# Performance work log

Measured on AMD Instinct MI355X. Metric: run time of the kernel, lower is better.

## Reference

```python
import jax, jax.numpy as jnp
import numpy as np
from jax.ops import segment_sum, segment_max

N, H, E, NEXP, K, L, HEADS, NM = 384, 768, 12288, 8, 2, 3, 4, 38
GAMMA, LAMBDA_SPD = 2.0, 0.5


def _ln(x, g, b, eps=1e-5):
    m = jnp.mean(x, -1, keepdims=True)
    v = jnp.mean((x - m) ** 2, -1, keepdims=True)
    return (x - m) / jnp.sqrt(v + eps) * g + b


def _gelu(x):
    return jax.nn.gelu(x, approximate=False)


def setup_inputs() -> dict:
    key = jax.random.key(0)
    ks = jax.random.split(key, 20)
    r = lambda i, sh: jax.random.normal(ks[i], sh, jnp.float32) * 0.02
    z = lambda sh: jnp.zeros(sh, jnp.float32)
    o = lambda sh: jnp.ones(sh, jnp.float32)
    return dict(
        feat_text=jax.random.normal(ks[0], (N, H), jnp.float32),
        feat_image=jax.random.normal(ks[1], (N, H), jnp.float32),
        spd_matrix=jax.random.uniform(ks[2], (N, N), dtype=jnp.float32),
        src=jax.random.randint(ks[3], (E,), 0, N, jnp.int32),
        dst=jax.random.randint(ks[4], (E,), 0, N, jnp.int32),
        mask_idx=jax.random.randint(ks[5], (NM,), 0, N, jnp.int32),
        mask_token=r(6, (H,)),
        gate_W=r(7, (H, NEXP)), gate_b=z((NEXP,)),
        exp_W1=r(8, (NEXP, H, H)), exp_b1=z((NEXP, H)),
        exp_g1=o((NEXP, H)), exp_be1=z((NEXP, H)),
        exp_W2=r(9, (NEXP, H, H)), exp_b2=z((NEXP, H)),
        gat_W=r(10, (L, H, HEADS * H)), gat_al=r(11, (L, HEADS, H)),
        gat_ar=r(12, (L, HEADS, H)), gat_b=z((L, HEADS * H)),
        dec_W1=r(13, (2, H, H)), dec_b1=z((2, H)),
        dec_g=o((2, H)), dec_be=z((2, H)),
        dec_W2=r(14, (2, H, H)), dec_b2=z((2, H)),
        spd_W1=r(15, (2 * H, H)), spd_b1=z((H,)),
        spd_g=o((H,)), spd_be=z((H,)),
        spd_W2=r(16, (H, 1)), spd_b2=z((1,)),
    )


def _forward(feat_text, feat_image, spd_matrix, mask_token, gate_W, gate_b,
             exp_W1, exp_b1, exp_g1, exp_be1, exp_W2, exp_b2,
             gat_W, gat_al, gat_ar, gat_b,
             dec_W1, dec_b1, dec_g, dec_be, dec_W2, dec_b2,
             spd_W1, spd_b1, spd_g, spd_be, spd_W2, spd_b2,
             src, dst, mask_idx):
    # mean of domain features, then mask-token replacement at fixed indices
    x = (feat_text + feat_image) * 0.5
    xm = x.at[mask_idx].set(mask_token)

    # --- MoE (all experts computed densely, top-2 gathered, as in source) ---
    gw = jax.nn.softmax(xm @ gate_W + gate_b, axis=-1)              # [N,NEXP]
    topw, topi = jax.lax.top_k(gw, K)
    topw = topw / jnp.sum(topw, -1, keepdims=True)
    eh = _gelu(_ln(jnp.einsum('nd,edh->neh', xm, exp_W1) + exp_b1, exp_g1, exp_be1))
    eo = jnp.einsum('neh,ehk->nek', eh, exp_W2) + exp_b2            # [N,NEXP,H]
    sel = jnp.take_along_axis(eo, topi[:, :, None], axis=1)          # [N,K,H]
    h = jnp.sum(sel * topw[:, :, None], axis=1)                      # [N,H]

    # --- stacked GATConv layers (DGL semantics), head-mean after each ---
    for l in range(L):
        f = (h @ gat_W[l]).reshape(N, HEADS, H)                      # [N,heads,H]
        el = jnp.sum(f * gat_al[l], -1)                              # [N,heads]
        er = jnp.sum(f * gat_ar[l], -1)
        e = jax.nn.leaky_relu(el[src] + er[dst], 0.2)                # [E,heads]
        emax = segment_max(e, dst, num_segments=N)
        emax = jnp.where(jnp.isfinite(emax), emax, 0.0)
        ex = jnp.exp(e - emax[dst])
        den = segment_sum(ex, dst, num_segments=N)
        alpha = ex / jnp.maximum(den[dst], 1e-9)                     # edge softmax by dst
        rst = segment_sum(alpha[:, :, None] * f[src], dst, num_segments=N)
        h = jnp.mean(rst + gat_b[l].reshape(HEADS, H), axis=1)       # [N,H]

    # --- domain reconstruction loss on masked nodes ---
    hm = h[mask_idx]
    feats = (feat_text, feat_image)
    recon = jnp.float32(0.0)
    for d in range(2):
        zz = _gelu(_ln(hm @ dec_W1[d] + dec_b1[d], dec_g[d], dec_be[d]))
        rec = zz @ dec_W2[d] + dec_b2[d]
        orig = feats[d][mask_idx]
        denom = jnp.maximum(jnp.linalg.norm(rec, axis=-1) * jnp.linalg.norm(orig, axis=-1), 1e-8)
        cos = jnp.sum(rec * orig, -1) / denom
        recon = recon + jnp.mean((1.0 - cos) ** GAMMA)

    # --- SPD loss over all N^2 pairs, vectorized ---
    # concat([h_i, h_j]) @ W1 == h_i @ W1[:H] + h_j @ W1[H:]  (exact decomposition)
    pa = h @ spd_W1[:H]                                              # [N,H]
    pb = h @ spd_W1[H:]                                              # [N,H]
    zp = _gelu(_ln(pa[:, None, :] + pb[None, :, :] + spd_b1, spd_g, spd_be))  # [N,N,H]
    pred = (zp @ spd_W2)[..., 0] + spd_b2[0]                         # [N,N]
    spd_loss = jnp.mean((pred - spd_matrix) ** 2)

    total = recon + LAMBDA_SPD * spd_loss
    return total, h


def reference(feat_text, feat_image, spd_matrix, src, dst, mask_idx, mask_token,
              gate_W, gate_b, exp_W1, exp_b1, exp_g1, exp_be1, exp_W2, exp_b2,
              gat_W, gat_al, gat_ar, gat_b,
              dec_W1, dec_b1, dec_g, dec_be, dec_W2, dec_b2,
              spd_W1, spd_b1, spd_g, spd_be, spd_W2, spd_b2):
    return _forward(feat_text, feat_image, spd_matrix, mask_token, gate_W, gate_b,
                    exp_W1, exp_b1, exp_g1, exp_be1, exp_W2, exp_b2,
                    gat_W, gat_al, gat_ar, gat_b,
                    dec_W1, dec_b1, dec_g, dec_be, dec_W2, dec_b2,
                    spd_W1, spd_b1, spd_g, spd_be, spd_W2, spd_b2,
                    src, dst, mask_idx)
```

## Files before the change

kernel.cpp:

```cpp
#include <hip/hip_runtime.h>
#include <hip/hip_bf16.h>
#include <math.h>

#define NN 384
#define HD 768
#define EE 12288
#define NCHUNK (EE / 256)
#define NEXPERT 8
#define TOPK 2
#define NLAYER 3
#define NHEADS 4
#define NMASK 38

typedef __attribute__((ext_vector_type(8))) short short8v;
typedef __attribute__((ext_vector_type(4))) float f32x4;
typedef __attribute__((ext_vector_type(2))) float f32x2;
typedef __attribute__((ext_vector_type(4))) int int4v;

__device__ __forceinline__ float gelu_f(float x) {
    return x * 0.5f * (1.f + erff(x * 0.70710678118654752440f));
}

__device__ __forceinline__ ushort f2bf(float x) {
    unsigned u = __float_as_uint(x);
    u += 0x7fffu + ((u >> 16) & 1u);
    return (ushort)(u >> 16);
}

__global__ __launch_bounds__(256) void k_xm_gate(const float* __restrict__ a,
        const float* __restrict__ b, const int* __restrict__ mask_idx,
        const float* __restrict__ mt, ushort* __restrict__ xm_bf,
        const float* __restrict__ gW, const float* __restrict__ gb,
        int* __restrict__ topi, float* __restrict__ topw) {
    int n = blockIdx.x, tid = threadIdx.x;
    __shared__ float xs[HD];
    __shared__ int ism;
    __shared__ float logits[NEXPERT];
    if (tid == 0) ism = 0;
    __syncthreads();
    if (tid < NMASK && mask_idx[tid] == n) ism = 1;
    __syncthreads();
#pragma unroll
    for (int r = 0; r < 3; r++) {
        int j = r * 256 + tid;
        float v = ism ? mt[j] : 0.5f * (a[(size_t)n * HD + j] + b[(size_t)n * HD + j]);
        xs[j] = v;
        xm_bf[(size_t)n * HD + j] = f2bf(v);
    }
    __syncthreads();
    int grp = tid >> 5;
    int l32 = tid & 31;
    float p = 0.f;
    for (int dd = l32; dd < HD; dd += 32) p += xs[dd] * gW[dd * NEXPERT + grp];
#pragma unroll
    for (int m = 1; m < 32; m <<= 1) p += __shfl_xor(p, m, 32);
    if (l32 == 0) logits[grp] = p + gb[grp];
    __syncthreads();
    if (tid == 0) {
        float mx = logits[0];
#pragma unroll
        for (int e = 1; e < NEXPERT; e++) mx = fmaxf(mx, logits[e]);
        float sm[NEXPERT]; float s = 0.f;
#pragma unroll
        for (int e = 0; e < NEXPERT; e++) { sm[e] = expf(logits[e] - mx); s += sm[e]; }
#pragma unroll
        for (int e = 0; e < NEXPERT; e++) sm[e] /= s;
        int i0 = 0; float b0 = sm[0];
#pragma unroll
        for (int e = 1; e < NEXPERT; e++) if (sm[e] > b0) { b0 = sm[e]; i0 = e; }
        int i1 = -1; float b1v = -1.f;
#pragma unroll
        for (int e = 0; e < NEXPERT; e++) if (e != i0 && sm[e] > b1v) { b1v = sm[e]; i1 = e; }
        float ssum = b0 + b1v;
        topi[n * 2] = i0; topi[n * 2 + 1] = i1;
        topw[n * 2] = b0 / ssum; topw[n * 2 + 1] = b1v / ssum;
    }
}

__global__ __launch_bounds__(256) void k_transpose_all(
        const float* __restrict__ w1, const float* __restrict__ w2,
        const float* __restrict__ gw, const float* __restrict__ sw,
        const float* __restrict__ dw1, const float* __restrict__ dw2,
        ushort* __restrict__ o1, ushort* __restrict__ o2, ushort* __restrict__ og,
        ushort* __restrict__ os, ushort* __restrict__ od1, ushort* __restrict__ od2) {
    int b = blockIdx.x;
    const float* src; ushort* dst; int N, loc, tilesX;
    if (b < 4608)       { src = w1;  dst = o1;  N = HD;     loc = b;         tilesX = 24; }
    else if (b < 9216)  { src = w2;  dst = o2;  N = HD;     loc = b - 4608;  tilesX = 24; }
    else if (b < 16128) { src = gw;  dst = og;  N = 4 * HD; loc = b - 9216;  tilesX = 96; }
    else if (b < 17280) { src = sw;  dst = os;  N = HD;     loc = b - 16128; tilesX = 24; }
    else if (b < 18432) { src = dw1; dst = od1; N = HD;     loc = b - 17280; tilesX = 24; }
    else                { src = dw2; dst = od2; N = HD;     loc = b - 18432; tilesX = 24; }
    const int K = HD;
    int tilesPerZ = tilesX * 24;
    int z = loc / tilesPerZ;
    int rem = loc - z * tilesPerZ;
    int ty = rem / tilesX, tx = rem - ty * tilesX;
    const float* inz = src + (size_t)z * K * N;
    ushort* outz = dst + (size_t)z * K * N;
    int n0 = tx * 32, k0 = ty * 32;

    __shared__ float t[32][36];
    int r = threadIdx.x >> 3, c4 = (threadIdx.x & 7) * 4;
    float4 v = *reinterpret_cast<const float4*>(inz + (size_t)(k0 + r) * N + n0 + c4);
    t[r][c4] = v.x; t[r][c4 + 1] = v.y; t[r][c4 + 2] = v.z; t[r][c4 + 3] = v.w;
    __syncthreads();
    int orow = n0 + r;
    uint2 p;
    ushort b0 = f2bf(t[c4 + 0][r]);
    ushort b1 = f2bf(t[c4 + 1][r]);
    ushort b2 = f2bf(t[c4 + 2][r]);
    ushort b3 = f2bf(t[c4 + 3][r]);
    p.x = (unsigned)b0 | ((unsigned)b1 << 16);
    p.y = (unsigned)b2 | ((unsigned)b3 << 16);
    *reinterpret_cast<uint2*>(outz + (size_t)orow * K + k0 + c4) = p;
}

__global__ __launch_bounds__(256) void k_moe_meta(const int* __restrict__ topi,
        int* __restrict__ ecnt, int* __restrict__ estart, int* __restrict__ posArr,
        int* __restrict__ eofpos, int* __restrict__ rowlist, int* __restrict__ dec_rs) {
    __shared__ int ti[NN * TOPK];
    __shared__ int cnt[NEXPERT];
    __shared__ int est[NEXPERT + 1];
    int tid = threadIdx.x;
    if (tid < NEXPERT) cnt[tid] = 0;
    __syncthreads();
    for (int a = tid; a < NN * TOPK; a += 256) ti[a] = topi[a];
    __syncthreads();
    for (int a = tid; a < NN * TOPK; a += 256) atomicAdd(&cnt[ti[a]], 1);
    __syncthreads();
    if (tid == 0) {
        int s = 0;
        for (int e = 0; e < NEXPERT; e++) { est[e] = s; s += cnt[e]; }
        est[NEXPERT] = s;
        dec_rs[0] = 0; dec_rs[1] = NMASK;
    }
    __syncthreads();
    if (tid < NEXPERT) { ecnt[tid] = cnt[tid]; estart[tid] = est[tid]; }
    if (tid == 0) estart[NEXPERT] = est[NEXPERT];
    for (int a = tid; a < NN * TOPK; a += 256) {
        int e = ti[a]; int rank = 0;
        for (int a2 = 0; a2 < a; a2++) rank += (ti[a2] == e) ? 1 : 0;
        int p = est[e] + rank;
        posArr[a] = p; eofpos[p] = e; rowlist[p] = a >> 1;
    }
}

__global__ __launch_bounds__(256) void k_hist(const int* __restrict__ dst,
                                              int* __restrict__ counts) {
    __shared__ int h[NN];
    int c = blockIdx.x;
    for (int i = threadIdx.x; i < NN; i += 256) h[i] = 0;
    __syncthreads();
    atomicAdd(&h[dst[c * 256 + threadIdx.x]], 1);
    __syncthreads();
    for (int i = threadIdx.x; i < NN; i += 256) counts[c * NN + i] = h[i];
}

__global__ __launch_bounds__(NN) void k_scan_all(const int* __restrict__ counts,
        int* __restrict__ chunkbase, int* __restrict__ nstart) {
    __shared__ int tot[NN];
    int n = threadIdx.x;
    int s = 0;
    for (int c = 0; c < NCHUNK; c++) { chunkbase[c * NN + n] = s; s += counts[c * NN + n]; }
    tot[n] = s;
    __syncthreads();
    for (int off = 1; off < NN; off <<= 1) {
        int v = tot[n];
        int add = (n >= off) ? tot[n - off] : 0;
        __syncthreads();
        tot[n] = v + add;
        __syncthreads();
    }
    nstart[n + 1] = tot[n];
    if (n == 0) nstart[0] = 0;
}

__global__ __launch_bounds__(256) void k_rank2(const int* __restrict__ dst,
        const int* __restrict__ chunkbase, const int* __restrict__ nstart,
        int* __restrict__ esorted) {
    __shared__ int ds[256];
    int c = blockIdx.x;
    int e = c * 256 + threadIdx.x;
    int d = dst[e];
    ds[threadIdx.x] = d;
    __syncthreads();
    int r = 0;
    for (int i = 0; i < threadIdx.x; i++) r += (ds[i] == d) ? 1 : 0;
    esorted[nstart[d] + chunkbase[c * NN + d] + r] = e;
}

__device__ __forceinline__ short8v ldfrag(const ushort* s, int r, int kb) {
    int c = kb ^ (r & 7);
    return *reinterpret_cast<const short8v*>(s + r * 64 + c * 8);
}

__global__ __launch_bounds__(256) void k_mfma_gemm(
        const ushort* __restrict__ A, const ushort* __restrict__ Bt, float* __restrict__ C,
        int M, int K, int lda, int ldc, long strideBt, long strideC,
        const int* __restrict__ rowsA, const int* __restrict__ Ms,
        const int* __restrict__ rowStarts) {
    int z = blockIdx.z;
    int Meff = Ms ? Ms[z] : M;
    int row0 = blockIdx.y * 64;
    if (row0 >= Meff) return;
    int col0 = blockIdx.x * 64;
    int rowbase = rowStarts ? rowStarts[z] : 0;
    const ushort* Btz = Bt + (size_t)z * strideBt;
    float* Cz = C + (size_t)rowbase * ldc + (size_t)z * strideC;
    const int* rz = rowsA ? (rowsA + rowbase) : nullptr;

    __shared__ ushort Asm[64 * 64];
    __shared__ ushort Bsm[64 * 64];

    int tid = threadIdx.x;
    int w = tid >> 6, lane = tid & 63;
    int wr = w >> 1, wc = w & 1;
    int l15 = lane & 15, lq = lane >> 4;

    f32x4 acc[2][2];
#pragma unroll
    for (int i = 0; i < 2; i++)
#pragma unroll
        for (int j = 0; j < 2; j++) acc[i][j] = (f32x4){0.f, 0.f, 0.f, 0.f};

    for (int k0 = 0; k0 < K; k0 += 64) {
#pragma unroll
        for (int ii = 0; ii < 2; ii++) {
            int i = tid + ii * 256;
            int r = i >> 3, c = i & 7;
            int cs = c ^ (r & 7);
            int4v av = (int4v){0, 0, 0, 0};
            int grow = row0 + r;
            if (grow < Meff) {
                int srow = rz ? rz[grow] : (rowbase + grow);
                av = *reinterpret_cast<const int4v*>(A + (size_t)srow * lda + k0 + c * 8);
            }
            *reinterpret_cast<int4v*>(&Asm[r * 64 + cs * 8]) = av;
            int4v bv = *reinterpret_cast<const int4v*>(Btz + (size_t)(col0 + r) * K + k0 + c * 8);
            *reinterpret_cast<int4v*>(&Bsm[r * 64 + cs * 8]) = bv;
        }
        __syncthreads();
#pragma unroll
        for (int ks = 0; ks < 2; ks++) {
            int kb = ks * 4 + lq;
            short8v a0 = ldfrag(Asm, wr * 32 + l15, kb);
            short8v a1 = ldfrag(Asm, wr * 32 + 16 + l15, kb);
            short8v b0 = ldfrag(Bsm, wc * 32 + l15, kb);
            short8v b1 = ldfrag(Bsm, wc * 32 + 16 + l15, kb);
            acc[0][0] = __builtin_amdgcn_mfma_f32_16x16x32_bf16(a0, b0, acc[0][0], 0, 0, 0);
            acc[0][1] = __builtin_amdgcn_mfma_f32_16x16x32_bf16(a0, b1, acc[0][1], 0, 0, 0);
            acc[1][0] = __builtin_amdgcn_mfma_f32_16x16x32_bf16(a1, b0, acc[1][0], 0, 0, 0);
            acc[1][1] = __builtin_amdgcn_mfma_f32_16x16x32_bf16(a1, b1, acc[1][1], 0, 0, 0);
        }
        __syncthreads();
    }
#pragma unroll
    for (int ai = 0; ai < 2; ai++)
#pragma unroll
        for (int bi = 0; bi < 2; bi++) {
            int rbase = row0 + wr * 32 + ai * 16 + (lq << 2);
            int cc = col0 + wc * 32 + bi * 16 + l15;
#pragma unroll
            for (int r = 0; r < 4; r++) {
                int rr = rbase + r;
                if (rr < Meff) Cz[(size_t)rr * ldc + cc] = acc[ai][bi][r];
            }
        }
}

__global__ __launch_bounds__(256) void k_ln_gelu(const float* __restrict__ t1,
        ushort* __restrict__ ehb, const float* __restrict__ b1, const float* __restrict__ g,
        const float* __restrict__ be, const int* __restrict__ eofpos) {
    int row = blockIdx.x;
    int e = eofpos[row];
    int tid = threadIdx.x;
    __shared__ float rA[4], rB[4];
    float v[3]; float s1 = 0.f, s2 = 0.f;
#pragma unroll
    for (int r = 0; r < 3; r++) {
        int c = r * 256 + tid;
        float x = t1[(size_t)row * HD + c] + b1[e * HD + c];
        v[r] = x; s1 += x; s2 += x * x;
    }
#pragma unroll
    for (int m = 1; m < 64; m <<= 1) { s1 += __shfl_xor(s1, m); s2 += __shfl_xor(s2, m); }
    int wave = tid >> 6, lane = tid & 63;
    if (lane == 0) { rA[wave] = s1; rB[wave] = s2; }
    __syncthreads();
    float S1 = rA[0] + rA[1] + rA[2] + rA[3];
    float S2 = rB[0] + rB[1] + rB[2] + rB[3];
    float mean = S1 * (1.f / HD);
    float var = S2 * (1.f / HD) - mean * mean;
    float rstd = rsqrtf(var + 1e-5f);
#pragma unroll
    for (int r = 0; r < 3; r++) {
        int c = r * 256 + tid;
        float zn = (v[r] - mean) * rstd * g[e * HD + c] + be[e * HD + c];
        ehb[(size_t)row * HD + c] = f2bf(gelu_f(zn));
    }
}

__global__ void k_combine_moe(const float* __restrict__ eo, const float* __restrict__ b2,
        const int* __restrict__ topi, const float* __restrict__ topw,
        const int* __restrict__ posArr, float* __restrict__ h, ushort* __restrict__ hb) {
    int n = blockIdx.x;
    int tid = threadIdx.x;
    int e0 = topi[n * 2], e1 = topi[n * 2 + 1];
    float w0 = topw[n * 2], w1 = topw[n * 2 + 1];
    int p0 = posArr[n * 2], p1 = posArr[n * 2 + 1];
    for (int j = tid; j < HD; j += 256) {
        float v0 = eo[(size_t)p0 * HD + j] + b2[e0 * HD + j];
        float v1 = eo[(size_t)p1 * HD + j] + b2[e1 * HD + j];
        float hv = w0 * v0 + w1 * v1;
        h[(size_t)n * HD + j] = hv;
        hb[(size_t)n * HD + j] = f2bf(hv);
    }
}

__global__ __launch_bounds__(256) void k_el_er(const float* __restrict__ f,
        const float* __restrict__ al, const float* __restrict__ ar,
        float* __restrict__ el, float* __restrict__ er) {
    int n = blockIdx.x;
    int hd = threadIdx.x >> 6, lane = threadIdx.x & 63;
    const float* fr = f + ((size_t)n * NHEADS + hd) * HD;
    float pl = 0.f, pr = 0.f;
    for (int j = lane; j < HD; j += 64) {
        float fv = fr[j];
        pl += fv * al[hd * HD + j];
        pr += fv * ar[hd * HD + j];
    }
#pragma unroll
    for (int m = 1; m < 64; m <<= 1) { pl += __shfl_xor(pl, m); pr += __shfl_xor(pr, m); }
    if (lane == 0) { el[n * NHEADS + hd] = pl; er[n * NHEADS + hd] = pr; }
}

__global__ __launch_bounds__(256) void k_gat_agg(const float* __restrict__ f,
        const float* __restrict__ el, const float* __restrict__ er,
        const int* __restrict__ src, const int* __restrict__ esorted,
        const int* __restrict__ nstart, const float* __restrict__ gb,
        float* __restrict__ hout, ushort* __restrict__ hb) {
    int n = blockIdx.x;
    int s0 = nstart[n], cnt = nstart[n + 1] - s0;
    int tid = threadIdx.x;
    __shared__ float red[4][NHEADS];
    __shared__ float emax_s[NHEADS], den_s[NHEADS];
    __shared__ float alpha_s[256][NHEADS];
    __shared__ int sn_s[256];
    float ern[NHEADS];
#pragma unroll
    for (int hd = 0; hd < NHEADS; hd++) ern[hd] = er[n * NHEADS + hd];
    int wave = tid >> 6, lane = tid & 63;

    float mx[NHEADS] = { -1e30f, -1e30f, -1e30f, -1e30f };
    for (int t = tid; t < cnt; t += 256) {
        int e = esorted[s0 + t]; int sn = src[e];
#pragma unroll
        for (int hd = 0; hd < NHEADS; hd++) {
            float v = el[sn * NHEADS + hd] + ern[hd];
            v = (v >= 0.f) ? v : 0.2f * v;
            mx[hd] = fmaxf(mx[hd], v);
        }
    }
#pragma unroll
    for (int hd = 0; hd < NHEADS; hd++) {
#pragma unroll
        for (int m = 1; m < 64; m <<= 1) mx[hd] = fmaxf(mx[hd], __shfl_xor(mx[hd], m));
    }
    if (lane == 0) { for (int hd = 0; hd < NHEADS; hd++) red[wave][hd] = mx[hd]; }
    __syncthreads();
    if (tid == 0) {
#pragma unroll
        for (int hd = 0; hd < NHEADS; hd++)
            emax_s[hd] = fmaxf(fmaxf(red[0][hd], red[1][hd]), fmaxf(red[2][hd], red[3][hd]));
    }
    __syncthreads();
    float sm[NHEADS] = { 0.f, 0.f, 0.f, 0.f };
    for (int t = tid; t < cnt; t += 256) {
        int e = esorted[s0 + t]; int sn = src[e];
#pragma unroll
        for (int hd = 0; hd < NHEADS; hd++) {
            float v = el[sn * NHEADS + hd] + ern[hd];
            v = (v >= 0.f) ? v : 0.2f * v;
            sm[hd] += expf(v - emax_s[hd]);
        }
    }
#pragma unroll
    for (int hd = 0; hd < NHEADS; hd++) {
#pragma unroll
        for (int m = 1; m < 64; m <<= 1) sm[hd] += __shfl_xor(sm[hd], m);
    }
    __syncthreads();
    if (lane == 0) { for (int hd = 0; hd < NHEADS; hd++) red[wave][hd] = sm[hd]; }
    __syncthreads();
    if (tid == 0) {
#pragma unroll
        for (int hd = 0; hd < NHEADS; hd++)
            den_s[hd] = red[0][hd] + red[1][hd] + red[2][hd] + red[3][hd];
    }
    __syncthreads();
    float acc[NHEADS][3] = {};
    for (int c0 = 0; c0 < cnt; c0 += 256) {
        int t = c0 + tid;
        if (t < cnt) {
            int e = esorted[s0 + t]; int sn = src[e];
            sn_s[tid] = sn;
#pragma unroll
            for (int hd = 0; hd < NHEADS; hd++) {
                float v = el[sn * NHEADS + hd] + ern[hd];
                v = (v >= 0.f) ? v : 0.2f * v;
                alpha_s[tid][hd] = expf(v - emax_s[hd]) / fmaxf(den_s[hd], 1e-9f);
            }
        }
        __syncthreads();
        int cm = cnt - c0; if (cm > 256) cm = 256;
        for (int i = 0; i < cm; i++) {
            int sn = sn_s[i];
            const float* fr = f + (size_t)sn * (NHEADS * HD);
#pragma unroll
            for (int hd = 0; hd < NHEADS; hd++) {
                float a = alpha_s[i][hd];
#pragma unroll
                for (int r = 0; r < 3; r++) acc[hd][r] += a * fr[hd * HD + r * 256 + tid];
            }
        }
        __syncthreads();
    }
#pragma unroll
    for (int r = 0; r < 3; r++) {
        int j = r * 256 + tid;
        float s = 0.f;
#pragma unroll
        for (int hd = 0; hd < NHEADS; hd++) s += acc[hd][r] + gb[hd * HD + j];
        float hv = 0.25f * s;
        hout[(size_t)n * HD + j] = hv;
        hb[(size_t)n * HD + j] = f2bf(hv);
    }
}

__global__ __launch_bounds__(256) void k_ln_gelu_dec(const float* __restrict__ t1,
        ushort* __restrict__ zzb, const float* __restrict__ b1, const float* __restrict__ g,
        const float* __restrict__ be) {
    int m = blockIdx.x, d = blockIdx.y;
    int row = d * NMASK + m;
    int tid = threadIdx.x;
    __shared__ float rA[4], rB[4];
    float v[3]; float s1 = 0.f, s2 = 0.f;
#pragma unroll
    for (int r = 0; r < 3; r++) {
        int c = r * 256 + tid;
        float x = t1[(size_t)row * HD + c] + b1[d * HD + c];
        v[r] = x; s1 += x; s2 += x * x;
    }
#pragma unroll
    for (int mm = 1; mm < 64; mm <<= 1) { s1 += __shfl_xor(s1, mm); s2 += __shfl_xor(s2, mm); }
    int wave = tid >> 6, lane = tid & 63;
    if (lane == 0) { rA[wave] = s1; rB[wave] = s2; }
    __syncthreads();
    float S1 = rA[0] + rA[1] + rA[2] + rA[3];
    float S2 = rB[0] + rB[1] + rB[2] + rB[3];
    float mean = S1 * (1.f / HD);
    float var = S2 * (1.f / HD) - mean * mean;
    float rstd = rsqrtf(var + 1e-5f);
#pragma unroll
    for (int r = 0; r < 3; r++) {
        int c = r * 256 + tid;
        float zn = (v[r] - mean) * rstd * g[d * HD + c] + be[d * HD + c];
        zzb[(size_t)row * HD + c] = f2bf(gelu_f(zn));
    }
}

__global__ __launch_bounds__(256) void k_cos(const float* __restrict__ rec,
        const float* __restrict__ b2, const int* __restrict__ mask_idx,
        const float* __restrict__ ft, const float* __restrict__ fi,
        float* __restrict__ rec_part) {
    int b = blockIdx.x;
    int d = b / NMASK, m = b % NMASK;
    int node = mask_idx[m];
    int tid = threadIdx.x;
    __shared__ float rA[4], rB[4], rC[4];
    const float* rrow = rec + (size_t)b * HD;
    const float* orig = (d == 0 ? ft : fi) + (size_t)node * HD;
    float pro = 0.f, prr = 0.f, poo = 0.f;
#pragma unroll
    for (int r = 0; r < 3; r++) {
        int c = r * 256 + tid;
        float rv = rrow[c] + b2[d * HD + c];
        float o = orig[c];
        pro += rv * o; prr += rv * rv; poo += o * o;
    }
#pragma unroll
    for (int mm = 1; mm < 64; mm <<= 1) {
        pro += __shfl_xor(pro, mm); prr += __shfl_xor(prr, mm); poo += __shfl_xor(poo, mm);
    }
    int wave = tid >> 6, lane = tid & 63;
    if (lane == 0) { rA[wave] = pro; rB[wave] = prr; rC[wave] = poo; }
    __syncthreads();
    if (tid == 0) {
        float P = rA[0] + rA[1] + rA[2] + rA[3];
        float R = rB[0] + rB[1] + rB[2] + rB[3];
        float O = rC[0] + rC[1] + rC[2] + rC[3];
        float denom = fmaxf(sqrtf(R) * sqrtf(O), 1e-8f);
        float cosv = P / denom;
        float t = 1.f - cosv;
        rec_part[b] = (t * t) * (1.f / (float)NMASK);
    }
}

__global__ __launch_bounds__(256) void k_spd_prep(float* __restrict__ pab,
        const float* __restrict__ b1, ushort* __restrict__ pp_bf,
        float* __restrict__ Svec, float* __restrict__ Qvec) {
    int r = blockIdx.x, tid = threadIdx.x;
    bool isA = r < NN;
    float* row = pab + (size_t)r * HD;
    __shared__ float rA[4], rB[4];
    float vv[3]; float s1 = 0.f, s2 = 0.f;
#pragma unroll
    for (int rr = 0; rr < 3; rr++) {
        int j = rr * 256 + tid;
        float v = row[j];
        if (isA) v += b1[j];
        vv[rr] = v; s1 += v; s2 += v * v;
    }
#pragma unroll
    for (int m = 1; m < 64; m <<= 1) { s1 += __shfl_xor(s1, m); s2 += __shfl_xor(s2, m); }
    int wave = tid >> 6, lane = tid & 63;
    if (lane == 0) { rA[wave] = s1; rB[wave] = s2; }
#pragma unroll
    for (int rr = 0; rr < 3; rr++) {
        int j = rr * 256 + tid;
        if (isA) row[j] = vv[rr];
        pp_bf[(size_t)r * HD + j] = f2bf(vv[rr]);
    }
    __syncthreads();
    if (tid == 0) {
        Svec[r] = rA[0] + rA[1] + rA[2] + rA[3];
        Qvec[r] = rB[0] + rB[1] + rB[2] + rB[3];
    }
}

#define GC1 2.3022085f
#define GC2 0.10294429f
__global__ __launch_bounds__(256) void k_spd2(const float* __restrict__ pab,
        const float* __restrict__ Svec, const float* __restrict__ Qvec,
        const float* __restrict__ cross, const float* __restrict__ g,
        const float* __restrict__ be, const float* __restrict__ w2,
        const float* __restrict__ b2, const float* __restrict__ spd,
        float* __restrict__ partials) {
    __shared__ f32x2 pa_s[HD / 2], g_s[HD / 2], be_s[HD / 2], w2_s[HD / 2];
    __shared__ float wsum[4];
    int i = blockIdx.x;
    const f32x2* paP = reinterpret_cast<const f32x2*>(pab + (size_t)i * HD);
    const f32x2* gP = reinterpret_cast<const f32x2*>(g);
    const f32x2* beP = reinterpret_cast<const f32x2*>(be);
    const f32x2* w2P = reinterpret_cast<const f32x2*>(w2);
    for (int t = threadIdx.x; t < HD / 2; t += 256) {
        pa_s[t] = paP[t];
        g_s[t] = gP[t]; be_s[t] = beP[t]; w2_s[t] = w2P[t];
    }
    __syncthreads();
    int wave = threadIdx.x >> 6, lane = threadIdx.x & 63;
    float Sa = Svec[i], Qa = Qvec[i];
    float bacc = 0.f;
    float b2v = b2[0];
    for (int j = blockIdx.y * 4 + wave; j < NN; j += 32) {
        const f32x2* pbj = reinterpret_cast<const f32x2*>(pab + (size_t)(NN + j) * HD);
        float mean = (Sa + Svec[NN + j]) * (1.f / HD);
        float ex2 = (Qa + Qvec[NN + j] + 2.f * cross[(size_t)i * NN + j]) * (1.f / HD);
        float var = ex2 - mean * mean;
        float rstd = rsqrtf(var + 1e-5f);
        f32x2 rstd2 = (f32x2){rstd, rstd};
        float nmr = -mean * rstd;
        f32x2 nmr2 = (f32x2){nmr, nmr};
        f32x2 dot2 = (f32x2){0.f, 0.f};
#pragma unroll
        for (int r = 0; r < 6; r++) {
            int e = r * 64 + lane;
            f32x2 z = pa_s[e] + pbj[e];
            f32x2 u = z * rstd2 + nmr2;
            f32x2 zn = u * g_s[e] + be_s[e];
            f32x2 t2 = zn * zn;
            f32x2 p = t2 * (f32x2){GC2, GC2} + (f32x2){GC1, GC1};
            f32x2 ua = zn * p;
            float e0 = __builtin_amdgcn_exp2f(-ua.x);
            float e1 = __builtin_amdgcn_exp2f(-ua.y);
            f32x2 rr = (f32x2){__builtin_amdgcn_rcpf(1.f + e0),
                               __builtin_amdgcn_rcpf(1.f + e1)};
            f32x2 gl = zn * rr;
            dot2 = gl * w2_s[e] + dot2;
        }
        float dot = dot2.x + dot2.y;
#pragma unroll
        for (int m = 1; m < 64; m <<= 1) dot += __shfl_xor(dot, m);
        if (lane == 0) {
            float d = (dot + b2v) - spd[(size_t)i * NN + j];
            bacc += d * d;
        }
    }
    if (lane == 0) wsum[wave] = bacc;
    __syncthreads();
    if (threadIdx.x == 0) partials[i * 8 + blockIdx.y] = wsum[0] + wsum[1] + wsum[2] + wsum[3];
}

__global__ __launch_bounds__(256) void k_out(const float* __restrict__ h,
        const float* __restrict__ rec_part, const float* __restrict__ spd_part,
        float* __restrict__ out) {
    if (blockIdx.x < NN * HD / 256) {
        int i = blockIdx.x * 256 + threadIdx.x;
        out[1 + i] = h[i];
        return;
    }
    __shared__ float rA[4], rB[4];
    int tid = threadIdx.x;
    float sp = 0.f, rc = 0.f;
    for (int t = tid; t < 8 * NN; t += 256) sp += spd_part[t];
    for (int t = tid; t < 2 * NMASK; t += 256) rc += rec_part[t];
#pragma unroll
    for (int m = 1; m < 64; m <<= 1) { sp += __shfl_xor(sp, m); rc += __shfl_xor(rc, m); }
    int wave = tid >> 6, lane = tid & 63;
    if (lane == 0) { rA[wave] = sp; rB[wave] = rc; }
    __syncthreads();
    if (tid == 0) {
        float SP = rA[0] + rA[1] + rA[2] + rA[3];
        float RC = rB[0] + rB[1] + rB[2] + rB[3];
        out[0] = RC + 0.5f * (SP * (1.f / ((float)NN * (float)NN)));
    }
}

extern "C" void kernel_launch(void* const* d_in, const int* in_sizes, int n_in,
                              void* d_out, int out_size, void* d_ws, size_t ws_size,
                              hipStream_t stream) {
    const float* feat_text = (const float*)d_in[0];
    const float* feat_image = (const float*)d_in[1];
    const float* spd_matrix = (const float*)d_in[2];
    const int*   src       = (const int*)d_in[3];
    const int*   dst       = (const int*)d_in[4];
    const int*   mask_idx  = (const int*)d_in[5];
    const float* mask_token = (const float*)d_in[6];
    const float* gate_W = (const float*)d_in[7];
    const float* gate_b = (const float*)d_in[8];
    const float* exp_W1 = (const float*)d_in[9];
    const float* exp_b1 = (const float*)d_in[10];
    const float* exp_g1 = (const float*)d_in[11];
    const float* exp_be1 = (const float*)d_in[12];
    const float* exp_W2 = (const float*)d_in[13];
    const float* exp_b2 = (const float*)d_in[14];
    const float* gat_W  = (const float*)d_in[15];
    const float* gat_al = (const float*)d_in[16];
    const float* gat_ar = (const float*)d_in[17];
    const float* gat_b  = (const float*)d_in[18];
    const float* dec_W1 = (const float*)d_in[19];
    const float* dec_b1 = (const float*)d_in[20];
    const float* dec_g  = (const float*)d_in[21];
    const float* dec_be = (const float*)d_in[22];
    const float* dec_W2 = (const float*)d_in[23];
    const float* dec_b2 = (const float*)d_in[24];
    const float* spd_W1 = (const float*)d_in[25];
    const float* spd_b1 = (const float*)d_in[26];
    const float* spd_g  = (const float*)d_in[27];
    const float* spd_be = (const float*)d_in[28];
    const float* spd_W2 = (const float*)d_in[29];
    const float* spd_b2 = (const float*)d_in[30];
    (void)in_sizes; (void)n_in; (void)ws_size; (void)out_size;

    float* ws = (float*)d_ws;
    size_t off = 0;
    auto alloc = [&](size_t nfl) { float* p = ws + off; off += (nfl + 3) & ~(size_t)3; return p; };
    float* hA   = alloc((size_t)NN * HD);
    float* hB   = alloc((size_t)NN * HD);
    float* t1   = alloc((size_t)NN * TOPK * HD);
    float* eo   = alloc((size_t)NN * TOPK * HD);
    float* fbuf = alloc((size_t)NN * NHEADS * HD);
    float* el   = alloc(NN * NHEADS);
    float* er   = alloc(NN * NHEADS);
    float* pab  = alloc((size_t)2 * NN * HD);
    float* cross = alloc((size_t)NN * NN);
    float* Svec = alloc(2 * NN);
    float* Qvec = alloc(2 * NN);
    float* topw = alloc(NN * TOPK);
    float* rec_part = alloc(2 * NMASK + 4);
    float* spd_part = alloc(8 * NN);
    int* topi    = (int*)alloc(NN * TOPK);
    int* ecnt    = (int*)alloc(16);
    int* estart  = (int*)alloc(16);
    int* posArr  = (int*)alloc(NN * TOPK);
    int* eofpos  = (int*)alloc(NN * TOPK);
    int* rowlist = (int*)alloc(NN * TOPK);
    int* dec_rs  = (int*)alloc(4);
    int* nstart  = (int*)alloc(NN + 4);
    int* esorted = (int*)alloc(EE);
    int* counts    = (int*)alloc((size_t)NCHUNK * NN);
    int* chunkbase = (int*)alloc((size_t)NCHUNK * NN);
    ushort* xm_bf  = (ushort*)alloc((size_t)NN * HD / 2);
    ushort* eh_bf  = (ushort*)alloc((size_t)NN * TOPK * HD / 2);
    ushort* hA_bf  = (ushort*)alloc((size_t)NN * HD / 2);
    ushort* hB_bf  = (ushort*)alloc((size_t)NN * HD / 2);
    ushort* pp_bf  = (ushort*)alloc((size_t)2 * NN * HD / 2);
    ushort* expW1t = (ushort*)alloc((size_t)NEXPERT * HD * HD / 2);
    ushort* expW2t = (ushort*)alloc((size_t)NEXPERT * HD * HD / 2);
    ushort* gatWt  = (ushort*)alloc((size_t)NLAYER * NHEADS * HD * HD / 2);
    ushort* spdW1t = (ushort*)alloc((size_t)2 * HD * HD / 2);
    ushort* decW1t = (ushort*)alloc((size_t)2 * HD * HD / 2);
    ushort* decW2t = (ushort*)alloc((size_t)2 * HD * HD / 2);

    k_transpose_all<<<dim3(19584), dim3(256), 0, stream>>>(
        exp_W1, exp_W2, gat_W, spd_W1, dec_W1, dec_W2,
        expW1t, expW2t, gatWt, spdW1t, decW1t, decW2t);

    k_xm_gate<<<dim3(NN), dim3(256), 0, stream>>>(
        feat_text, feat_image, mask_idx, mask_token, xm_bf, gate_W, gate_b, topi, topw);
    k_moe_meta<<<dim3(1), dim3(256), 0, stream>>>(topi, ecnt, estart, posArr, eofpos,
                                                  rowlist, dec_rs);

    k_hist<<<dim3(NCHUNK), dim3(256), 0, stream>>>(dst, counts);
    k_scan_all<<<dim3(1), dim3(NN), 0, stream>>>(counts, chunkbase, nstart);
    k_rank2<<<dim3(NCHUNK), dim3(256), 0, stream>>>(dst, chunkbase, nstart, esorted);

    k_mfma_gemm<<<dim3(HD / 64, 12, NEXPERT), dim3(256), 0, stream>>>(
        xm_bf, expW1t, t1, 0, HD, HD, HD, (long)HD * HD, 0, rowlist, ecnt, estart);
    k_ln_gelu<<<dim3(NN * TOPK), dim3(256), 0, stream>>>(t1, eh_bf, exp_b1, exp_g1, exp_be1, eofpos);
    k_mfma_gemm<<<dim3(HD / 64, 12, NEXPERT), dim3(256), 0, stream>>>(
        eh_bf, expW2t, eo, 0, HD, HD, HD, (long)HD * HD, 0, nullptr, ecnt, estart);
    k_combine_moe<<<dim3(NN), dim3(256), 0, stream>>>(eo, exp_b2, topi, topw, posArr, hA, hA_bf);

    float* hcur = hA; float* hnxt = hB;
    ushort* hcur_bf = hA_bf; ushort* hnxt_bf = hB_bf;
    for (int l = 0; l < NLAYER; l++) {
        k_mfma_gemm<<<dim3(NHEADS * HD / 64, NN / 64, 1), dim3(256), 0, stream>>>(
            hcur_bf, gatWt + (size_t)l * NHEADS * HD * HD, fbuf,
            NN, HD, HD, NHEADS * HD, 0, 0, nullptr, nullptr, nullptr);
        k_el_er<<<dim3(NN), dim3(256), 0, stream>>>(
            fbuf, gat_al + (size_t)l * NHEADS * HD, gat_ar + (size_t)l * NHEADS * HD, el, er);
        k_gat_agg<<<dim3(NN), dim3(256), 0, stream>>>(
            fbuf, el, er, src, esorted, nstart, gat_b + (size_t)l * NHEADS * HD, hnxt, hnxt_bf);
        float* t = hcur; hcur = hnxt; hnxt = t;
        ushort* tb = hcur_bf; hcur_bf = hnxt_bf; hnxt_bf = tb;
    }

    k_mfma_gemm<<<dim3(HD / 64, 1, 2), dim3(256), 0, stream>>>(
        hcur_bf, decW1t, t1, NMASK, HD, HD, HD, (long)HD * HD, (long)NMASK * HD,
        mask_idx, nullptr, nullptr);
    k_ln_gelu_dec<<<dim3(NMASK, 2), dim3(256), 0, stream>>>(t1, eh_bf, dec_b1, dec_g, dec_be);
    k_mfma_gemm<<<dim3(HD / 64, 1, 2), dim3(256), 0, stream>>>(
        eh_bf, decW2t, eo, NMASK, HD, HD, HD, (long)HD * HD, 0,
        nullptr, nullptr, dec_rs);
    k_cos<<<dim3(2 * NMASK), dim3(256), 0, stream>>>(
        eo, dec_b2, mask_idx, feat_text, feat_image, rec_part);

    k_mfma_gemm<<<dim3(HD / 64, NN / 64, 2), dim3(256), 0, stream>>>(
        hcur_bf, spdW1t, pab, NN, HD, HD, HD, (long)HD * HD, (long)NN * HD,
        nullptr, nullptr, nullptr);
    k_spd_prep<<<dim3(2 * NN), dim3(256), 0, stream>>>(pab, spd_b1, pp_bf, Svec, Qvec);
    k_mfma_gemm<<<dim3(NN / 64, NN / 64, 1), dim3(256), 0, stream>>>(
        pp_bf, pp_bf + (size_t)NN * HD, cross, NN, HD, HD, NN, 0, 0,
        nullptr, nullptr, nullptr);
    k_spd2<<<dim3(NN, 8), dim3(256), 0, stream>>>(
        pab, Svec, Qvec, cross, spd_g, spd_be, spd_W2, spd_b2, spd_matrix, spd_part);

    k_out<<<dim3(NN * HD / 256 + 1), dim3(256), 0, stream>>>(
        hcur, rec_part, spd_part, (float*)d_out);
}
```

Baseline: 361.1 us.

## Restructure SPD pairwise kernel to thread-per-pair with transposed pb, use direct global-to-LDS loads in GEMM

The SPD pairwise GELU/LN kernel is rewritten so that each thread handles one (i,j) pair and iterates over the hidden dimension. It reads a transposed copy of pb written by the prep kernel, which gives coalesced column loads, and reads pa, gamma, beta and w2 packed as float4 from LDS. This replaces the per-pair wave reduction with one lane-level accumulation, removing the cross-lane shuffles per pair. The MFMA GEMM tile loads now use global_load_lds to copy straight into LDS, skipping the register staging. Out-of-range rows are clamped to Meff-1 instead of zero-filled. This adds an extra transposed buffer write.

```diff
diff --git a/kernel.cpp b/kernel.cpp
--- a/kernel.cpp
+++ b/kernel.cpp
@@ -14,7 +14,6 @@
 
 typedef __attribute__((ext_vector_type(8))) short short8v;
 typedef __attribute__((ext_vector_type(4))) float f32x4;
-typedef __attribute__((ext_vector_type(2))) float f32x2;
 typedef __attribute__((ext_vector_type(4))) int int4v;
 
 __device__ __forceinline__ float gelu_f(float x) {
@@ -25,6 +24,12 @@
     unsigned u = __float_as_uint(x);
     u += 0x7fffu + ((u >> 16) & 1u);
     return (ushort)(u >> 16);
+}
+
+__device__ __forceinline__ void gload_lds16(const void* g, void* l) {
+    __builtin_amdgcn_global_load_lds(
+        (const __attribute__((address_space(1))) void*)g,
+        (__attribute__((address_space(3))) void*)l, 16, 0, 0);
 }
 
 __global__ __launch_bounds__(256) void k_xm_gate(const float* __restrict__ a,
@@ -218,6 +223,7 @@
     int wr = w >> 1, wc = w & 1;
     int l15 = lane & 15, lq = lane >> 4;
 
+    int r0s = tid >> 3, c0s = tid & 7;
     f32x4 acc[2][2];
 #pragma unroll
     for (int i = 0; i < 2; i++)
@@ -227,18 +233,15 @@
     for (int k0 = 0; k0 < K; k0 += 64) {
 #pragma unroll
         for (int ii = 0; ii < 2; ii++) {
-            int i = tid + ii * 256;
-            int r = i >> 3, c = i & 7;
-            int cs = c ^ (r & 7);
-            int4v av = (int4v){0, 0, 0, 0};
+            int r = r0s + ii * 32;
+            int cs = c0s ^ (r & 7);
             int grow = row0 + r;
-            if (grow < Meff) {
-                int srow = rz ? rz[grow] : (rowbase + grow);
-                av = *reinterpret_cast<const int4v*>(A + (size_t)srow * lda + k0 + c * 8);
-            }
-            *reinterpret_cast<int4v*>(&Asm[r * 64 + cs * 8]) = av;
-            int4v bv = *reinterpret_cast<const int4v*>(Btz + (size_t)(col0 + r) * K + k0 + c * 8);
-            *reinterpret_cast<int4v*>(&Bsm[r * 64 + cs * 8]) = bv;
+            int gc = (grow < Meff) ? grow : (Meff - 1);
+            int srow = rz ? rz[gc] : (rowbase + gc);
+            ushort* ldsA = &Asm[(size_t)(w * 8 + ii * 32) * 64];
+            ushort* ldsB = &Bsm[(size_t)(w * 8 + ii * 32) * 64];
+            gload_lds16(A + (size_t)srow * lda + k0 + cs * 8, ldsA);
+            gload_lds16(Btz + (size_t)(col0 + r) * K + k0 + cs * 8, ldsB);
         }
         __syncthreads();
 #pragma unroll
@@ -509,7 +512,7 @@
 
 __global__ __launch_bounds__(256) void k_spd_prep(float* __restrict__ pab,
         const float* __restrict__ b1, ushort* __restrict__ pp_bf,
-        float* __restrict__ Svec, float* __restrict__ Qvec) {
+        float* __restrict__ Svec, float* __restrict__ Qvec, float* __restrict__ pbT) {
     int r = blockIdx.x, tid = threadIdx.x;
     bool isA = r < NN;
     float* row = pab + (size_t)r * HD;
@@ -530,6 +533,7 @@
     for (int rr = 0; rr < 3; rr++) {
         int j = rr * 256 + tid;
         if (isA) row[j] = vv[rr];
+        else pbT[(size_t)j * NN + (r - NN)] = vv[rr];
         pp_bf[(size_t)r * HD + j] = f2bf(vv[rr]);
     }
     __syncthreads();
@@ -541,65 +545,61 @@
 
 #define GC1 2.3022085f
 #define GC2 0.10294429f
-__global__ __launch_bounds__(256) void k_spd2(const float* __restrict__ pab,
-        const float* __restrict__ Svec, const float* __restrict__ Qvec,
-        const float* __restrict__ cross, const float* __restrict__ g,
-        const float* __restrict__ be, const float* __restrict__ w2,
-        const float* __restrict__ b2, const float* __restrict__ spd,
-        float* __restrict__ partials) {
-    __shared__ f32x2 pa_s[HD / 2], g_s[HD / 2], be_s[HD / 2], w2_s[HD / 2];
-    __shared__ float wsum[4];
+__device__ __forceinline__ float gfast(float zn) {
+    float ua = zn * fmaf(zn * zn, GC2, GC1);
+    float e = __builtin_amdgcn_exp2f(-ua);
+    return zn * __builtin_amdgcn_rcpf(1.f + e);
+}
+
+__global__ __launch_bounds__(384) void k_spdj(const float* __restrict__ pab,
+        const float* __restrict__ pbT, const float* __restrict__ Svec,
+        const float* __restrict__ Qvec, const float* __restrict__ cross,
+        const float* __restrict__ g, const float* __restrict__ be,
+        const float* __restrict__ w2, const float* __restrict__ b2,
+        const float* __restrict__ spd, float* __restrict__ partials) {
     int i = blockIdx.x;
-    const f32x2* paP = reinterpret_cast<const f32x2*>(pab + (size_t)i * HD);
-    const f32x2* gP = reinterpret_cast<const f32x2*>(g);
-    const f32x2* beP = reinterpret_cast<const f32x2*>(be);
-    const f32x2* w2P = reinterpret_cast<const f32x2*>(w2);
-    for (int t = threadIdx.x; t < HD / 2; t += 256) {
-        pa_s[t] = paP[t];
-        g_s[t] = gP[t]; be_s[t] = beP[t]; w2_s[t] = w2P[t];
-    }
-    __syncthreads();
-    int wave = threadIdx.x >> 6, lane = threadIdx.x & 63;
+    int wv = threadIdx.x >> 6, lane = threadIdx.x & 63;
+    int j = threadIdx.x;
+    __shared__ __align__(16) float PG[HD][4];
+    for (int t = threadIdx.x; t < HD; t += 384) {
+        PG[t][0] = pab[(size_t)i * HD + t];
+        PG[t][1] = g[t];
+        PG[t][2] = be[t];
+        PG[t][3] = w2[t];
+    }
+    __syncthreads();
     float Sa = Svec[i], Qa = Qvec[i];
-    float bacc = 0.f;
-    float b2v = b2[0];
-    for (int j = blockIdx.y * 4 + wave; j < NN; j += 32) {
-        const f32x2* pbj = reinterpret_cast<const f32x2*>(pab + (size_t)(NN + j) * HD);
-        float mean = (Sa + Svec[NN + j]) * (1.f / HD);
-        float ex2 = (Qa + Qvec[NN + j] + 2.f * cross[(size_t)i * NN + j]) * (1.f / HD);
-        float var = ex2 - mean * mean;
-        float rstd = rsqrtf(var + 1e-5f);
-        f32x2 rstd2 = (f32x2){rstd, rstd};
-        float nmr = -mean * rstd;
-        f32x2 nmr2 = (f32x2){nmr, nmr};
-        f32x2 dot2 = (f32x2){0.f, 0.f};
-#pragma unroll
-        for (int r = 0; r < 6; r++) {
-            int e = r * 64 + lane;
-            f32x2 z = pa_s[e] + pbj[e];
-            f32x2 u = z * rstd2 + nmr2;
-            f32x2 zn = u * g_s[e] + be_s[e];
-            f32x2 t2 = zn * zn;
-            f32x2 p = t2 * (f32x2){GC2, GC2} + (f32x2){GC1, GC1};
-            f32x2 ua = zn * p;
-            float e0 = __builtin_amdgcn_exp2f(-ua.x);
-            float e1 = __builtin_amdgcn_exp2f(-ua.y);
-            f32x2 rr = (f32x2){__builtin_amdgcn_rcpf(1.f + e0),
-                               __builtin_amdgcn_rcpf(1.f + e1)};
-            f32x2 gl = zn * rr;
-            dot2 = gl * w2_s[e] + dot2;
-        }
-        float dot = dot2.x + dot2.y;
-#pragma unroll
-        for (int m = 1; m < 64; m <<= 1) dot += __shfl_xor(dot, m);
-        if (lane == 0) {
-            float d = (dot + b2v) - spd[(size_t)i * NN + j];
-            bacc += d * d;
-        }
-    }
-    if (lane == 0) wsum[wave] = bacc;
-    __syncthreads();
-    if (threadIdx.x == 0) partials[i * 8 + blockIdx.y] = wsum[0] + wsum[1] + wsum[2] + wsum[3];
+    float mean = (Sa + Svec[NN + j]) * (1.f / HD);
+    float ex2 = (Qa + Qvec[NN + j] + 2.f * cross[(size_t)i * NN + j]) * (1.f / HD);
+    float rstd = rsqrtf(ex2 - mean * mean + 1e-5f);
+    float nmr = -mean * rstd;
+    const float* pcol = pbT + j;
+    float d0 = 0.f, d1 = 0.f, d2 = 0.f, d3 = 0.f;
+#pragma unroll 2
+    for (int e = 0; e < HD; e += 4) {
+        float p0 = pcol[(size_t)(e + 0) * NN];
+        float p1 = pcol[(size_t)(e + 1) * NN];
+        float p2 = pcol[(size_t)(e + 2) * NN];
+        float p3 = pcol[(size_t)(e + 3) * NN];
+        float4 q0 = *reinterpret_cast<const float4*>(&PG[e + 0][0]);
+        float4 q1 = *reinterpret_cast<const float4*>(&PG[e + 1][0]);
+        float4 q2 = *reinterpret_cast<const float4*>(&PG[e + 2][0]);
+        float4 q3 = *reinterpret_cast<const float4*>(&PG[e + 3][0]);
+        float zn0 = fmaf(fmaf(q0.x + p0, rstd, nmr), q0.y, q0.z);
+        float zn1 = fmaf(fmaf(q1.x + p1, rstd, nmr), q1.y, q1.z);
+        float zn2 = fmaf(fmaf(q2.x + p2, rstd, nmr), q2.y, q2.z);
+        float zn3 = fmaf(fmaf(q3.x + p3, rstd, nmr), q3.y, q3.z);
+        d0 = fmaf(gfast(zn0), q0.w, d0);
+        d1 = fmaf(gfast(zn1), q1.w, d1);
+        d2 = fmaf(gfast(zn2), q2.w, d2);
+        d3 = fmaf(gfast(zn3), q3.w, d3);
+    }
+    float pred = ((d0 + d1) + (d2 + d3)) + b2[0];
+    float diff = pred - spd[(size_t)i * NN + j];
+    float sq = diff * diff;
+#pragma unroll
+    for (int m = 1; m < 64; m <<= 1) sq += __shfl_xor(sq, m);
+    if (lane == 0) partials[i * 6 + wv] = sq;
 }
 
 __global__ __launch_bounds__(256) void k_out(const float* __restrict__ h,
@@ -613,7 +613,7 @@
     __shared__ float rA[4], rB[4];
     int tid = threadIdx.x;
     float sp = 0.f, rc = 0.f;
-    for (int t = tid; t < 8 * NN; t += 256) sp += spd_part[t];
+    for (int t = tid; t < 6 * NN; t += 256) sp += spd_part[t];
     for (int t = tid; t < 2 * NMASK; t += 256) rc += rec_part[t];
 #pragma unroll
     for (int m = 1; m < 64; m <<= 1) { sp += __shfl_xor(sp, m); rc += __shfl_xor(rc, m); }
@@ -674,12 +674,13 @@
     float* el   = alloc(NN * NHEADS);
     float* er   = alloc(NN * NHEADS);
     float* pab  = alloc((size_t)2 * NN * HD);
+    float* pbT  = alloc((size_t)HD * NN);
     float* cross = alloc((size_t)NN * NN);
     float* Svec = alloc(2 * NN);
     float* Qvec = alloc(2 * NN);
     float* topw = alloc(NN * TOPK);
     float* rec_part = alloc(2 * NMASK + 4);
-    float* spd_part = alloc(8 * NN);
+    float* spd_part = alloc(6 * NN);
     int* topi    = (int*)alloc(NN * TOPK);
     int* ecnt    = (int*)alloc(16);
     int* estart  = (int*)alloc(16);
@@ -750,12 +751,12 @@
     k_mfma_gemm<<<dim3(HD / 64, NN / 64, 2), dim3(256), 0, stream>>>(
         hcur_bf, spdW1t, pab, NN, HD, HD, HD, (long)HD * HD, (long)NN * HD,
         nullptr, nullptr, nullptr);
-    k_spd_prep<<<dim3(2 * NN), dim3(256), 0, stream>>>(pab, spd_b1, pp_bf, Svec, Qvec);
+    k_spd_prep<<<dim3(2 * NN), dim3(256), 0, stream>>>(pab, spd_b1, pp_bf, Svec, Qvec, pbT);
     k_mfma_gemm<<<dim3(NN / 64, NN / 64, 1), dim3(256), 0, stream>>>(
         pp_bf, pp_bf + (size_t)NN * HD, cross, NN, HD, HD, NN, 0, 0,
         nullptr, nullptr, nullptr);
-    k_spd2<<<dim3(NN, 8), dim3(256), 0, stream>>>(
-        pab, Svec, Qvec, cross, spd_g, spd_be, spd_W2, spd_b2, spd_matrix, spd_part);
+    k_spdj<<<dim3(NN), dim3(384), 0, stream>>>(
+        pab, pbT, Svec, Qvec, cross, spd_g, spd_be, spd_W2, spd_b2, spd_matrix, spd_part);
 
     k_out<<<dim3(NN * HD / 256 + 1), dim3(256), 0, stream>>>(
         hcur, rec_part, spd_part, (float*)d_out);
```

Result: slower. 401.3 us (+11.1%).
